# Kernel optimization log

Measured on AMD Instinct MI355X. Metric: run time of the kernel, lower is better.

Reference implementation:

```python
import jax, jax.numpy as jnp
import numpy as np

TEMP = 0.1
COEFF = 0.5
WARMUP = 0
S = 32 * 32  # hardcoded in the torch module


def _l2n(x, axis):
    # matches F.normalize(p=2, eps=1e-12)
    n = jnp.linalg.norm(x, axis=axis, keepdims=True)
    return x / jnp.maximum(n, 1e-12)


def _ce_first_class(pos, neg):
    # cross-entropy with label 0 on logits = [pos | neg] / T
    logits = jnp.concatenate([pos, neg], axis=1) / TEMP
    return jnp.mean(jax.nn.logsumexp(logits, axis=1) - logits[:, 0])


def _dense_losses(q_of, q_x, k_of, k_x, k_avg_dense):
    # q_of,k_of: (B,d,S) normalized; q_x,k_x: (B,C,S) normalized; k_avg_dense: (B,C) UN-normalized (torch bug preserved)
    B, C, _ = q_x.shape
    sim = jnp.einsum('bds,bdt->bst', q_of, k_of)          # (B,S,S)
    ind = jnp.argmax(sim, axis=2)                          # (B,S)
    idxg = jnp.take_along_axis(k_x, jnp.broadcast_to(ind[:, None, :], k_x.shape), axis=2)
    idxg = jax.lax.stop_gradient(idxg)                     # computed under torch.no_grad
    l_pos = jnp.sum(q_x * idxg, axis=1).reshape(-1, 1)     # (B*S,1)
    qf = jnp.transpose(q_x, (0, 2, 1)).reshape(-1, C)      # (B*S,C)
    l_neg_full = qf @ k_avg_dense.T                        # (B*S,B)
    # static mask: row n excludes column n // S
    base = np.stack([np.delete(np.arange(B), i) for i in range(B)])  # (B,B-1)
    neg_cols = jnp.asarray(np.repeat(base, S, axis=0))     # (B*S,B-1)
    l_neg = jnp.take_along_axis(l_neg_full, neg_cols, axis=1)
    return l_pos, l_neg


def _forward(original_features_q, avgpooled_global_q, x_q, avgpooled_dense_q,
             original_features_k, avgpooled_global_k, x_k, avgpooled_dense_k, epoch):
    of = jnp.concatenate([original_features_q, original_features_k], axis=0)
    ag = jnp.concatenate([avgpooled_global_q, avgpooled_global_k], axis=0)
    x = jnp.concatenate([x_q, x_k], axis=0)
    ad = jnp.concatenate([avgpooled_dense_q, avgpooled_dense_k], axis=0)

    # global InfoNCE
    agn = _l2n(ag, 1)
    sim = agn @ agn.T                                      # (2B,2B)
    n2 = sim.shape[0]
    B = n2 // 2
    rows = np.arange(n2)
    pos_cols = (rows + B) % n2
    pos = sim[jnp.asarray(rows), jnp.asarray(pos_cols)][:, None]
    neg_cols = np.stack([np.setdiff1d(rows, [i, pos_cols[i]]) for i in range(n2)])  # (2B,2B-2)
    neg = jnp.take_along_axis(sim, jnp.asarray(neg_cols), axis=1)
    global_loss = _ce_first_class(pos, neg)

    # dense InfoNCE
    b, d, h, w = of.shape
    of = _l2n(of.reshape(b, d, h * w), 1)
    xn = _l2n(x, 1)
    q_of, k_of = of[:b // 2], of[b // 2:]
    q_x, k_x = xn[:b // 2], xn[b // 2:]
    q_ad, k_ad = ad[:b // 2], ad[b // 2:]  # NOTE: un-normalized, matching the torch code
    p1, n1 = _dense_losses(q_of, q_x, k_of, k_x, k_ad)
    p2, n2_ = _dense_losses(k_of, k_x, q_of, q_x, q_ad)
    dense_loss = _ce_first_class(jnp.concatenate([p1, p2], axis=0),
                                 jnp.concatenate([n1, n2_], axis=0))

    if epoch > WARMUP:
        return COEFF * global_loss + (1.0 - COEFF) * dense_loss
    return global_loss


def setup_inputs() -> dict:
    key = jax.random.key(0)
    ks = jax.random.split(key, 8)
    B, d, C, h, w = 64, 256, 128, 32, 32
    return {
        'original_features_q': jax.random.normal(ks[0], (B, d, h, w), jnp.float32),
        'avgpooled_global_q': jax.random.normal(ks[1], (B, C), jnp.float32),
        'x_q': jax.random.normal(ks[2], (B, C, h * w), jnp.float32),
        'avgpooled_dense_q': jax.random.normal(ks[3], (B, C), jnp.float32),
        'original_features_k': jax.random.normal(ks[4], (B, d, h, w), jnp.float32),
        'avgpooled_global_k': jax.random.normal(ks[5], (B, C), jnp.float32),
        'x_k': jax.random.normal(ks[6], (B, C, h * w), jnp.float32),
        'avgpooled_dense_k': jax.random.normal(ks[7], (B, C), jnp.float32),
        'epoch': 5,
    }


def reference(original_features_q, avgpooled_global_q, x_q, avgpooled_dense_q,
              original_features_k, avgpooled_global_k, x_k, avgpooled_dense_k, epoch):
    return _forward(original_features_q, avgpooled_global_q, x_q, avgpooled_dense_q,
                    original_features_k, avgpooled_global_k, x_k, avgpooled_dense_k, epoch)
```

## Files before the change

### kernel.cpp

```cpp
#include <hip/hip_runtime.h>
#include <math.h>

#define TEMP_INV 10.0f

typedef unsigned long long u64;
typedef __attribute__((ext_vector_type(8))) __bf16 bf16x8;
typedef __attribute__((ext_vector_type(4))) float f32x4;

__device__ inline unsigned fkey(float v) {
  unsigned u = __float_as_uint(v);
  return (u & 0x80000000u) ? ~u : (u | 0x80000000u);
}
__device__ inline u64 packvi(float v, unsigned idx) {
  return ((u64)fkey(v) << 32) | (u64)(0xFFFFFFFFu - idx);
}

__device__ __forceinline__ void async_copy16(const void* gp, void* lp) {
  __builtin_amdgcn_global_load_lds(
      (__attribute__((address_space(1))) void*)(unsigned long long)gp,
      (__attribute__((address_space(3))) void*)(unsigned long long)lp,
      16, 0, 0);
}

__global__ __launch_bounds__(256) void kcvt(const float* __restrict__ ofq,
                                            const float* __restrict__ ofk,
                                            __bf16* __restrict__ ofT,
                                            float* __restrict__ of_invn) {
  int s0 = blockIdx.x * 32, b = blockIdx.y;
  const float* src = (b < 64) ? (ofq + (size_t)b * 262144) : (ofk + (size_t)(b - 64) * 262144);
  __shared__ __bf16 T[32][36];
  __shared__ float R[8][32];
  int t = threadIdx.x;
  int dd = t >> 5, ss = t & 31;
  int wr = t >> 3, wd = t & 7;
  float ssq = 0.f;
  __bf16* out = ofT + (size_t)b * 262144 + (size_t)s0 * 256;
  for (int d0 = 0; d0 < 256; d0 += 32) {
    float v[4];
#pragma unroll
    for (int it = 0; it < 4; ++it) {
      int d = d0 + dd + 8 * it;
      v[it] = src[(size_t)d * 1024 + s0 + ss];
      ssq += v[it] * v[it];
    }
    __syncthreads();
#pragma unroll
    for (int it = 0; it < 4; ++it) T[ss][dd + 8 * it] = (__bf16)v[it];
    __syncthreads();
    *(uint2*)(out + (size_t)wr * 256 + d0 + wd * 4) = *(const uint2*)(&T[wr][wd * 4]);
  }
  R[dd][ss] = ssq;
  __syncthreads();
  if (t < 32) {
    float a = 0.f;
#pragma unroll
    for (int r = 0; r < 8; ++r) a += R[r][t];
    of_invn[b * 1024 + s0 + t] = 1.0f / fmaxf(sqrtf(a), 1e-12f);
  }
}

__global__ void kprep(const float* __restrict__ xq, const float* __restrict__ xk,
                      float* __restrict__ x_invn,
                      const float* __restrict__ adq, const float* __restrict__ adk,
                      float* __restrict__ adt) {
  if (blockIdx.x < 512) {
    int idx = blockIdx.x * 256 + threadIdx.x;
    int b = idx >> 10, s = idx & 1023;
    const float* src = (b < 64) ? (xq + (size_t)b * 131072) : (xk + (size_t)(b - 64) * 131072);
    float acc = 0.f;
#pragma unroll 8
    for (int c = 0; c < 128; ++c) { float v = src[c * 1024 + s]; acc += v * v; }
    x_invn[idx] = 1.0f / fmaxf(sqrtf(acc), 1e-12f);
  } else {
    int i = (blockIdx.x - 512) * 256 + threadIdx.x;
    int dir = i >> 13, r = i & 8191;
    int j = r >> 7, c = r & 127;
    const float* ad = dir == 0 ? adk : adq;
    adt[dir * 8192 + c * 64 + j] = ad[j * 128 + c];
  }
}

__global__ __launch_bounds__(256) void ksim(
    const __bf16* __restrict__ ofT, const float* __restrict__ of_invn,
    u64* __restrict__ best_row, u64* __restrict__ best_col) {
  int b = blockIdx.z;
  int s0 = blockIdx.x * 128, t0 = blockIdx.y * 128;
  const __bf16* Ag = ofT + (size_t)b * 262144;
  const __bf16* Bg = ofT + (size_t)(b + 64) * 262144;
  __shared__ __bf16 As[2][4096];
  __shared__ __bf16 Bs[2][4096];
  __shared__ float siq[128], sik[128];
  int t = threadIdx.x;
  if (t < 128) siq[t] = of_invn[b * 1024 + s0 + t];
  else sik[t - 128] = of_invn[65536 + b * 1024 + t0 + (t - 128)];

  f32x4 acc[4][4];
#pragma unroll
  for (int i = 0; i < 4; ++i)
#pragma unroll
    for (int j = 0; j < 4; ++j) acc[i][j] = (f32x4)(0.f);

  int lane = t & 63, w = t >> 6;
  int lc = lane & 15, q = lane >> 4;
  int wm = w & 1, wn = w >> 1;

  int aoff[4], boff[4];
#pragma unroll
  for (int i = 0; i < 4; ++i) {
    int mr = wm * 64 + i * 16 + lc;
    aoff[i] = mr * 32 + (((q + mr + (mr >> 2)) & 3) << 3);
    int nc = wn * 64 + i * 16 + lc;
    boff[i] = nc * 32 + (((q + nc + (nc >> 2)) & 3) << 3);
  }

  int kp = t & 3;
  int mA0 = t >> 2, lgA0 = (kp - mA0 - (mA0 >> 2)) & 3;
  int mA1 = 64 + (t >> 2), lgA1 = (kp - mA1 - (mA1 >> 2)) & 3;

  async_copy16(Ag + (size_t)(s0 + mA0) * 256 + lgA0 * 8, (char*)&As[0][0] + t * 16);
  async_copy16(Bg + (size_t)(t0 + mA0) * 256 + lgA0 * 8, (char*)&Bs[0][0] + t * 16);
  async_copy16(Ag + (size_t)(s0 + mA1) * 256 + lgA1 * 8, (char*)&As[0][0] + 4096 + t * 16);
  async_copy16(Bg + (size_t)(t0 + mA1) * 256 + lgA1 * 8, (char*)&Bs[0][0] + 4096 + t * 16);
  __syncthreads();

  for (int it = 0; it < 8; ++it) {
    int buf = it & 1;
    bf16x8 af[4], bfr[4];
#pragma unroll
    for (int i = 0; i < 4; ++i) af[i] = *(const bf16x8*)(&As[buf][0] + aoff[i]);
#pragma unroll
    for (int j = 0; j < 4; ++j) bfr[j] = *(const bf16x8*)(&Bs[buf][0] + boff[j]);
    if (it < 7) {
      int k0 = (it + 1) * 32;
      async_copy16(Ag + (size_t)(s0 + mA0) * 256 + k0 + lgA0 * 8, (char*)&As[buf ^ 1][0] + t * 16);
      async_copy16(Bg + (size_t)(t0 + mA0) * 256 + k0 + lgA0 * 8, (char*)&Bs[buf ^ 1][0] + t * 16);
      async_copy16(Ag + (size_t)(s0 + mA1) * 256 + k0 + lgA1 * 8, (char*)&As[buf ^ 1][0] + 4096 + t * 16);
      async_copy16(Bg + (size_t)(t0 + mA1) * 256 + k0 + lgA1 * 8, (char*)&Bs[buf ^ 1][0] + 4096 + t * 16);
    }
#pragma unroll
    for (int i = 0; i < 4; ++i)
#pragma unroll
      for (int j = 0; j < 4; ++j)
        acc[i][j] = __builtin_amdgcn_mfma_f32_16x16x32_bf16(af[i], bfr[j], acc[i][j], 0, 0, 0);
    __syncthreads();
  }

  float sk[4], sq[16];
#pragma unroll
  for (int j = 0; j < 4; ++j) sk[j] = sik[wn * 64 + j * 16 + lc];
#pragma unroll
  for (int i = 0; i < 4; ++i)
#pragma unroll
    for (int e = 0; e < 4; ++e) sq[i * 4 + e] = siq[wm * 64 + i * 16 + q * 4 + e];

  u64* browb = best_row + (size_t)b * 1024 + s0;
  u64* bcolb = best_col + (size_t)b * 1024 + t0;

#pragma unroll
  for (int i = 0; i < 4; ++i) {
#pragma unroll
    for (int e = 0; e < 4; ++e) {
      float v[4];
#pragma unroll
      for (int j = 0; j < 4; ++j) v[j] = acc[i][j][e] * sk[j];
      float vb = fmaxf(fmaxf(v[0], v[1]), fmaxf(v[2], v[3]));
#pragma unroll
      for (int mask = 1; mask <= 8; mask <<= 1) vb = fmaxf(vb, __shfl_xor(vb, mask));
      unsigned ib = 0xFFFFFFFFu;
#pragma unroll
      for (int j = 0; j < 4; ++j) {
        unsigned cand = (v[j] == vb) ? (unsigned)(t0 + wn * 64 + j * 16 + lc) : 0xFFFFFFFFu;
        ib = min(ib, cand);
      }
#pragma unroll
      for (int mask = 1; mask <= 8; mask <<= 1) ib = min(ib, __shfl_xor(ib, mask));
      if (lc == 0)
        atomicMax(browb + wm * 64 + i * 16 + q * 4 + e, ((u64)fkey(vb) << 32) | (u64)(0xFFFFFFFFu - ib));
    }
  }

#pragma unroll
  for (int j = 0; j < 4; ++j) {
    float cb = -INFINITY;
#pragma unroll
    for (int i = 0; i < 4; ++i)
#pragma unroll
      for (int e = 0; e < 4; ++e) cb = fmaxf(cb, acc[i][j][e] * sq[i * 4 + e]);
    cb = fmaxf(cb, __shfl_xor(cb, 16));
    cb = fmaxf(cb, __shfl_xor(cb, 32));
    unsigned ib = 0xFFFFFFFFu;
#pragma unroll
    for (int i = 0; i < 4; ++i)
#pragma unroll
      for (int e = 0; e < 4; ++e) {
        float m2 = acc[i][j][e] * sq[i * 4 + e];
        unsigned cand = (m2 == cb) ? (unsigned)(s0 + wm * 64 + i * 16 + q * 4 + e) : 0xFFFFFFFFu;
        ib = min(ib, cand);
      }
    ib = min(ib, __shfl_xor(ib, 16));
    ib = min(ib, __shfl_xor(ib, 32));
    if (lane < 16)
      atomicMax(bcolb + wn * 64 + j * 16 + lane, ((u64)fkey(cb) << 32) | (u64)(0xFFFFFFFFu - ib));
  }
}

__global__ __launch_bounds__(1024) void kpos(
    const float* __restrict__ xq, const float* __restrict__ xk,
    const float* __restrict__ x_invn,
    const u64* __restrict__ best_row, const u64* __restrict__ best_col,
    float* __restrict__ posl) {
  int b = blockIdx.x, dir = blockIdx.y;
  const float* xsrc = dir == 0 ? xq : xk;
  const float* xdst = dir == 0 ? xk : xq;
  const float* inv_src = x_invn + (dir ? 65536 : 0);
  const float* inv_dst = x_invn + (dir ? 0 : 65536);
  const u64* best = dir == 0 ? best_row : best_col;

  __shared__ float xrow[8][1024];
  __shared__ float sdinv[1024];
  int t = threadIdx.x;
  sdinv[t] = inv_dst[b * 1024 + t];
  u64 p = best[(size_t)b * 1024 + t];
  int sidx = (int)(0xFFFFFFFFu - (unsigned)(p & 0xFFFFFFFFull));
  const float* xsb = xsrc + (size_t)b * 131072;
  const float* xdb = xdst + (size_t)b * 131072;
  float acc = 0.f;
  for (int c0 = 0; c0 < 128; c0 += 8) {
    __syncthreads();
#pragma unroll
    for (int qq = 0; qq < 2; ++qq)
      ((float4*)xrow)[t + 1024 * qq] = ((const float4*)(xdb + (size_t)c0 * 1024))[t + 1024 * qq];
    __syncthreads();
#pragma unroll
    for (int cc = 0; cc < 8; ++cc)
      acc += xsb[(size_t)(c0 + cc) * 1024 + t] * xrow[cc][sidx];
  }
  posl[dir * 65536 + b * 1024 + t] = acc * inv_src[b * 1024 + t] * sdinv[sidx] * TEMP_INV;
}

__global__ __launch_bounds__(256) void kneg(
    const float* __restrict__ xq, const float* __restrict__ xk,
    const float* __restrict__ x_invn,
    const float* __restrict__ adt, const float* __restrict__ posl,
    float* __restrict__ dsum) {
  int st = blockIdx.x, b = blockIdx.y, dir = blockIdx.z;
  const float* xsrc = dir == 0 ? xq : xk;
  const float* inv_src = x_invn + (dir ? 65536 : 0);
  const float* Bt = adt + dir * 8192;

  __shared__ float As2[64][64];
  __shared__ float Bs2[128][64];
  __shared__ float red[16];

  int tid = threadIdx.x;
  int tx = tid & 15, ty = tid >> 4;
  int s0 = st * 64;

#pragma unroll
  for (int qq = 0; qq < 8; ++qq)
    reinterpret_cast<float4*>(Bs2)[tid + 256 * qq] =
        reinterpret_cast<const float4*>(Bt)[tid + 256 * qq];

  float acc[4][4];
#pragma unroll
  for (int i = 0; i < 4; ++i)
#pragma unroll
    for (int j = 0; j < 4; ++j) acc[i][j] = 0.f;

  int lm = tid & 63, lk = tid >> 6;
  float sinv = inv_src[b * 1024 + s0 + lm];
  const float* xb = xsrc + (size_t)b * 131072;

  for (int k0 = 0; k0 < 128; k0 += 64) {
#pragma unroll
    for (int r = 0; r < 16; ++r) {
      int kk = lk + 4 * r;
      As2[kk][lm] = xb[(k0 + kk) * 1024 + s0 + lm] * sinv;
    }
    __syncthreads();
#pragma unroll
    for (int kk = 0; kk < 64; ++kk) {
      float4 av = *reinterpret_cast<const float4*>(&As2[kk][ty * 4]);
      float4 bv = *reinterpret_cast<const float4*>(&Bs2[k0 + kk][tx * 4]);
      float a[4] = {av.x, av.y, av.z, av.w};
      float bb[4] = {bv.x, bv.y, bv.z, bv.w};
#pragma unroll
      for (int i = 0; i < 4; ++i)
#pragma unroll
        for (int j = 0; j < 4; ++j) acc[i][j] += a[i] * bb[j];
    }
    __syncthreads();
  }

  float lsum = 0.f;
#pragma unroll
  for (int i = 0; i < 4; ++i) {
    int s = s0 + ty * 4 + i;
    float pos = posl[dir * 65536 + b * 1024 + s];
    float lg[4];
    float mloc = -INFINITY;
#pragma unroll
    for (int j = 0; j < 4; ++j) {
      int jg = tx * 4 + j;
      lg[j] = (jg == b) ? -INFINITY : acc[i][j] * TEMP_INV;
      mloc = fmaxf(mloc, lg[j]);
    }
#pragma unroll
    for (int mask = 1; mask <= 8; mask <<= 1) mloc = fmaxf(mloc, __shfl_xor(mloc, mask));
    float m = fmaxf(mloc, pos);
    float e = 0.f;
#pragma unroll
    for (int j = 0; j < 4; ++j) e += __expf(lg[j] - m);
#pragma unroll
    for (int mask = 1; mask <= 8; mask <<= 1) e += __shfl_xor(e, mask);
    if (tx == 0) lsum += m + __logf(e + __expf(pos - m)) - pos;
  }
  if (tx == 0) red[ty] = lsum;
  __syncthreads();
  if (tid == 0) {
    float v = 0.f;
#pragma unroll
    for (int r = 0; r < 16; ++r) v += red[r];
    atomicAdd(dsum, v);
  }
}

__global__ void kglobal(const float* __restrict__ agq, const float* __restrict__ agk,
                        float* __restrict__ gsum) {
  __shared__ float logits[128];
  __shared__ float rinv[128];
  int i = blockIdx.x, j = threadIdx.x;
  const float* rowi = (i < 64) ? (agq + i * 128) : (agk + (i - 64) * 128);
  const float* rowj = (j < 64) ? (agq + j * 128) : (agk + (j - 64) * 128);
  float dot = 0.f, nj = 0.f;
#pragma unroll 8
  for (int c = 0; c < 128; ++c) { float a = rowi[c], bb = rowj[c]; dot += a * bb; nj += bb * bb; }
  rinv[j] = 1.0f / fmaxf(sqrtf(nj), 1e-12f);
  __syncthreads();
  logits[j] = dot * rinv[i] * rinv[j] * TEMP_INV;
  __syncthreads();
  if (j == 0) {
    int pos = (i + 64) & 127;
    float m = -INFINITY;
    for (int t = 0; t < 128; ++t) if (t != i) m = fmaxf(m, logits[t]);
    float e = 0.f;
    for (int t = 0; t < 128; ++t) if (t != i) e += __expf(logits[t] - m);
    atomicAdd(gsum, m + __logf(e) - logits[pos]);
  }
}

__global__ void kfinal(const float* __restrict__ gsum, const float* __restrict__ dsum,
                       const int* __restrict__ epoch, float* __restrict__ out) {
  if (threadIdx.x == 0) {
    float g = gsum[0] / 128.0f;
    float dn = dsum[0] / 131072.0f;
    out[0] = (epoch[0] > 0) ? (0.5f * g + 0.5f * dn) : g;
  }
}

extern "C" void kernel_launch(void* const* d_in, const int* in_sizes, int n_in,
                              void* d_out, int out_size, void* d_ws, size_t ws_size,
                              hipStream_t stream) {
  const float* ofq = (const float*)d_in[0];
  const float* agq = (const float*)d_in[1];
  const float* xq  = (const float*)d_in[2];
  const float* adq = (const float*)d_in[3];
  const float* ofk = (const float*)d_in[4];
  const float* agk = (const float*)d_in[5];
  const float* xk  = (const float*)d_in[6];
  const float* adk = (const float*)d_in[7];
  const int* epoch = (const int*)d_in[8];
  float* out = (float*)d_out;

  char* wsb = (char*)d_ws;
  __bf16* ofT = (__bf16*)wsb;
  u64* best_row = (u64*)(wsb + 67108864);
  u64* best_col = best_row + 65536;
  float* gsum = (float*)(best_col + 65536);
  float* dsum = gsum + 1;
  float* posl = dsum + 1;
  float* x_invn  = posl + 131072;
  float* of_invn = x_invn + 131072;
  float* adt = of_invn + 131072;

  hipMemsetAsync(best_row, 0, 65536ull * 8 * 2 + 8, stream);

  dim3 gc(32, 128);
  kcvt<<<gc, 256, 0, stream>>>(ofq, ofk, ofT, of_invn);
  kprep<<<576, 256, 0, stream>>>(xq, xk, x_invn, adq, adk, adt);
  kglobal<<<128, 128, 0, stream>>>(agq, agk, gsum);

  dim3 gs(8, 8, 64);
  ksim<<<gs, 256, 0, stream>>>(ofT, of_invn, best_row, best_col);

  dim3 gp(64, 2);
  kpos<<<gp, 1024, 0, stream>>>(xq, xk, x_invn, best_row, best_col, posl);

  dim3 gn(16, 64, 2);
  kneg<<<gn, 256, 0, stream>>>(xq, xk, x_invn, adt, posl, dsum);

  kfinal<<<1, 1, 0, stream>>>(gsum, dsum, epoch, out);
}
```

Measured before the change: 421.9 us.

## Enlarge similarity GEMM tiles to 256x256 with XOR-swizzled 64-wide K stages

```diff
diff --git a/kernel.cpp b/kernel.cpp
--- a/kernel.cpp
+++ b/kernel.cpp
@@ -10,9 +10,6 @@
 __device__ inline unsigned fkey(float v) {
   unsigned u = __float_as_uint(v);
   return (u & 0x80000000u) ? ~u : (u | 0x80000000u);
-}
-__device__ inline u64 packvi(float v, unsigned idx) {
-  return ((u64)fkey(v) << 32) | (u64)(0xFFFFFFFFu - idx);
 }
 
 __device__ __forceinline__ void async_copy16(const void* gp, void* lp) {
@@ -80,84 +77,94 @@
   }
 }
 
-__global__ __launch_bounds__(256) void ksim(
+__global__ __launch_bounds__(512, 2) void ksim(
     const __bf16* __restrict__ ofT, const float* __restrict__ of_invn,
     u64* __restrict__ best_row, u64* __restrict__ best_col) {
   int b = blockIdx.z;
-  int s0 = blockIdx.x * 128, t0 = blockIdx.y * 128;
+  int s0 = blockIdx.x * 256, t0 = blockIdx.y * 256;
   const __bf16* Ag = ofT + (size_t)b * 262144;
   const __bf16* Bg = ofT + (size_t)(b + 64) * 262144;
-  __shared__ __bf16 As[2][4096];
-  __shared__ __bf16 Bs[2][4096];
-  __shared__ float siq[128], sik[128];
+  __shared__ __bf16 As[2][16384];
+  __shared__ __bf16 Bs[2][16384];
+
   int t = threadIdx.x;
-  if (t < 128) siq[t] = of_invn[b * 1024 + s0 + t];
-  else sik[t - 128] = of_invn[65536 + b * 1024 + t0 + (t - 128)];
-
-  f32x4 acc[4][4];
-#pragma unroll
-  for (int i = 0; i < 4; ++i)
-#pragma unroll
-    for (int j = 0; j < 4; ++j) acc[i][j] = (f32x4)(0.f);
-
   int lane = t & 63, w = t >> 6;
   int lc = lane & 15, q = lane >> 4;
-  int wm = w & 1, wn = w >> 1;
-
-  int aoff[4], boff[4];
-#pragma unroll
-  for (int i = 0; i < 4; ++i) {
-    int mr = wm * 64 + i * 16 + lc;
-    aoff[i] = mr * 32 + (((q + mr + (mr >> 2)) & 3) << 3);
-    int nc = wn * 64 + i * 16 + lc;
-    boff[i] = nc * 32 + (((q + nc + (nc >> 2)) & 3) << 3);
-  }
-
-  int kp = t & 3;
-  int mA0 = t >> 2, lgA0 = (kp - mA0 - (mA0 >> 2)) & 3;
-  int mA1 = 64 + (t >> 2), lgA1 = (kp - mA1 - (mA1 >> 2)) & 3;
-
-  async_copy16(Ag + (size_t)(s0 + mA0) * 256 + lgA0 * 8, (char*)&As[0][0] + t * 16);
-  async_copy16(Bg + (size_t)(t0 + mA0) * 256 + lgA0 * 8, (char*)&Bs[0][0] + t * 16);
-  async_copy16(Ag + (size_t)(s0 + mA1) * 256 + lgA1 * 8, (char*)&As[0][0] + 4096 + t * 16);
-  async_copy16(Bg + (size_t)(t0 + mA1) * 256 + lgA1 * 8, (char*)&Bs[0][0] + 4096 + t * 16);
+  int wm = w >> 2, wn = w & 3;
+
+  f32x4 acc[8][4];
+#pragma unroll
+  for (int i = 0; i < 8; ++i)
+#pragma unroll
+    for (int j = 0; j < 4; ++j) acc[i][j] = (f32x4)(0.f);
+
+  int aoff[8], boff[4];
+#pragma unroll
+  for (int i = 0; i < 8; ++i) {
+    int mr = wm * 128 + i * 16 + lc;
+    aoff[i] = mr * 64 + ((q ^ (mr & 7)) << 3);
+  }
+#pragma unroll
+  for (int j = 0; j < 4; ++j) {
+    int nc = wn * 64 + j * 16 + lc;
+    boff[j] = nc * 64 + ((q ^ (nc & 7)) << 3);
+  }
+
+  int ms = t >> 3, gphys = t & 7;
+  int lg = gphys ^ (ms & 7);
+  size_t aSrc = (size_t)(s0 + ms) * 256 + lg * 8;
+  size_t bSrc = (size_t)(t0 + ms) * 256 + lg * 8;
+
+  auto STAGE = [&](int bufn, int k0) {
+    char* aL = (char*)&As[bufn][0] + t * 16;
+    char* bL = (char*)&Bs[bufn][0] + t * 16;
+#pragma unroll
+    for (int c = 0; c < 4; ++c) {
+      async_copy16(Ag + aSrc + (size_t)c * 16384 + k0, aL + c * 8192);
+      async_copy16(Bg + bSrc + (size_t)c * 16384 + k0, bL + c * 8192);
+    }
+  };
+
+  STAGE(0, 0);
   __syncthreads();
 
-  for (int it = 0; it < 8; ++it) {
+  for (int it = 0; it < 4; ++it) {
     int buf = it & 1;
-    bf16x8 af[4], bfr[4];
-#pragma unroll
-    for (int i = 0; i < 4; ++i) af[i] = *(const bf16x8*)(&As[buf][0] + aoff[i]);
-#pragma unroll
-    for (int j = 0; j < 4; ++j) bfr[j] = *(const bf16x8*)(&Bs[buf][0] + boff[j]);
-    if (it < 7) {
-      int k0 = (it + 1) * 32;
-      async_copy16(Ag + (size_t)(s0 + mA0) * 256 + k0 + lgA0 * 8, (char*)&As[buf ^ 1][0] + t * 16);
-      async_copy16(Bg + (size_t)(t0 + mA0) * 256 + k0 + lgA0 * 8, (char*)&Bs[buf ^ 1][0] + t * 16);
-      async_copy16(Ag + (size_t)(s0 + mA1) * 256 + k0 + lgA1 * 8, (char*)&As[buf ^ 1][0] + 4096 + t * 16);
-      async_copy16(Bg + (size_t)(t0 + mA1) * 256 + k0 + lgA1 * 8, (char*)&Bs[buf ^ 1][0] + 4096 + t * 16);
-    }
-#pragma unroll
-    for (int i = 0; i < 4; ++i)
-#pragma unroll
-      for (int j = 0; j < 4; ++j)
-        acc[i][j] = __builtin_amdgcn_mfma_f32_16x16x32_bf16(af[i], bfr[j], acc[i][j], 0, 0, 0);
-    __syncthreads();
-  }
-
-  float sk[4], sq[16];
-#pragma unroll
-  for (int j = 0; j < 4; ++j) sk[j] = sik[wn * 64 + j * 16 + lc];
-#pragma unroll
-  for (int i = 0; i < 4; ++i)
-#pragma unroll
-    for (int e = 0; e < 4; ++e) sq[i * 4 + e] = siq[wm * 64 + i * 16 + q * 4 + e];
+    if (it < 3) STAGE(buf ^ 1, (it + 1) * 64);
+#pragma unroll
+    for (int kk = 0; kk < 2; ++kk) {
+      int kx = kk << 5;
+      bf16x8 af[8], bfr[4];
+#pragma unroll
+      for (int i = 0; i < 8; ++i) af[i] = *(const bf16x8*)(&As[buf][0] + (aoff[i] ^ kx));
+#pragma unroll
+      for (int j = 0; j < 4; ++j) bfr[j] = *(const bf16x8*)(&Bs[buf][0] + (boff[j] ^ kx));
+      __builtin_amdgcn_s_setprio(1);
+#pragma unroll
+      for (int i = 0; i < 8; ++i)
+#pragma unroll
+        for (int j = 0; j < 4; ++j)
+          acc[i][j] = __builtin_amdgcn_mfma_f32_16x16x32_bf16(af[i], bfr[j], acc[i][j], 0, 0, 0);
+      __builtin_amdgcn_s_setprio(0);
+    }
+    __syncthreads();
+  }
+
+  float sk[4];
+#pragma unroll
+  for (int j = 0; j < 4; ++j) sk[j] = of_invn[65536 + b * 1024 + t0 + wn * 64 + j * 16 + lc];
+  float sq[32];
+#pragma unroll
+  for (int i = 0; i < 8; ++i)
+#pragma unroll
+    for (int e = 0; e < 4; ++e)
+      sq[i * 4 + e] = of_invn[b * 1024 + s0 + wm * 128 + i * 16 + q * 4 + e];
 
   u64* browb = best_row + (size_t)b * 1024 + s0;
   u64* bcolb = best_col + (size_t)b * 1024 + t0;
 
 #pragma unroll
-  for (int i = 0; i < 4; ++i) {
+  for (int i = 0; i < 8; ++i) {
 #pragma unroll
     for (int e = 0; e < 4; ++e) {
       float v[4];
@@ -175,7 +182,8 @@
 #pragma unroll
       for (int mask = 1; mask <= 8; mask <<= 1) ib = min(ib, __shfl_xor(ib, mask));
       if (lc == 0)
-        atomicMax(browb + wm * 64 + i * 16 + q * 4 + e, ((u64)fkey(vb) << 32) | (u64)(0xFFFFFFFFu - ib));
+        atomicMax(browb + wm * 128 + i * 16 + q * 4 + e,
+                  ((u64)fkey(vb) << 32) | (u64)(0xFFFFFFFFu - ib));
     }
   }
 
@@ -183,24 +191,25 @@
   for (int j = 0; j < 4; ++j) {
     float cb = -INFINITY;
 #pragma unroll
-    for (int i = 0; i < 4; ++i)
+    for (int i = 0; i < 8; ++i)
 #pragma unroll
       for (int e = 0; e < 4; ++e) cb = fmaxf(cb, acc[i][j][e] * sq[i * 4 + e]);
     cb = fmaxf(cb, __shfl_xor(cb, 16));
     cb = fmaxf(cb, __shfl_xor(cb, 32));
     unsigned ib = 0xFFFFFFFFu;
 #pragma unroll
-    for (int i = 0; i < 4; ++i)
+    for (int i = 0; i < 8; ++i)
 #pragma unroll
       for (int e = 0; e < 4; ++e) {
         float m2 = acc[i][j][e] * sq[i * 4 + e];
-        unsigned cand = (m2 == cb) ? (unsigned)(s0 + wm * 64 + i * 16 + q * 4 + e) : 0xFFFFFFFFu;
+        unsigned cand = (m2 == cb) ? (unsigned)(s0 + wm * 128 + i * 16 + q * 4 + e) : 0xFFFFFFFFu;
         ib = min(ib, cand);
       }
     ib = min(ib, __shfl_xor(ib, 16));
     ib = min(ib, __shfl_xor(ib, 32));
     if (lane < 16)
-      atomicMax(bcolb + wn * 64 + j * 16 + lane, ((u64)fkey(cb) << 32) | (u64)(0xFFFFFFFFu - ib));
+      atomicMax(bcolb + wn * 64 + j * 16 + lane,
+                ((u64)fkey(cb) << 32) | (u64)(0xFFFFFFFFu - ib));
   }
 }
 
@@ -390,8 +399,8 @@
   kprep<<<576, 256, 0, stream>>>(xq, xk, x_invn, adq, adk, adt);
   kglobal<<<128, 128, 0, stream>>>(agq, agk, gsum);
 
-  dim3 gs(8, 8, 64);
-  ksim<<<gs, 256, 0, stream>>>(ofT, of_invn, best_row, best_col);
+  dim3 gs(4, 4, 64);
+  ksim<<<gs, 512, 0, stream>>>(ofT, of_invn, best_row, best_col);
 
   dim3 gp(64, 2);
   kpos<<<gp, 1024, 0, stream>>>(xq, xk, x_invn, best_row, best_col, posl);
```

Measured after the change: 403.6 us. 1.05x faster.

## Load MFMA operands directly from global into registers, drop LDS staging in ksim

Applied to the files above, without the earlier changes.

```diff
diff --git a/kernel.cpp b/kernel.cpp
--- a/kernel.cpp
+++ b/kernel.cpp
@@ -10,16 +10,6 @@
 __device__ inline unsigned fkey(float v) {
   unsigned u = __float_as_uint(v);
   return (u & 0x80000000u) ? ~u : (u | 0x80000000u);
-}
-__device__ inline u64 packvi(float v, unsigned idx) {
-  return ((u64)fkey(v) << 32) | (u64)(0xFFFFFFFFu - idx);
-}
-
-__device__ __forceinline__ void async_copy16(const void* gp, void* lp) {
-  __builtin_amdgcn_global_load_lds(
-      (__attribute__((address_space(1))) void*)(unsigned long long)gp,
-      (__attribute__((address_space(3))) void*)(unsigned long long)lp,
-      16, 0, 0);
 }
 
 __global__ __launch_bounds__(256) void kcvt(const float* __restrict__ ofq,
@@ -80,78 +70,63 @@
   }
 }
 
-__global__ __launch_bounds__(256) void ksim(
+__global__ __launch_bounds__(256, 3) void ksim(
     const __bf16* __restrict__ ofT, const float* __restrict__ of_invn,
     u64* __restrict__ best_row, u64* __restrict__ best_col) {
   int b = blockIdx.z;
   int s0 = blockIdx.x * 128, t0 = blockIdx.y * 128;
   const __bf16* Ag = ofT + (size_t)b * 262144;
   const __bf16* Bg = ofT + (size_t)(b + 64) * 262144;
-  __shared__ __bf16 As[2][4096];
-  __shared__ __bf16 Bs[2][4096];
-  __shared__ float siq[128], sik[128];
+
   int t = threadIdx.x;
-  if (t < 128) siq[t] = of_invn[b * 1024 + s0 + t];
-  else sik[t - 128] = of_invn[65536 + b * 1024 + t0 + (t - 128)];
-
-  f32x4 acc[4][4];
-#pragma unroll
-  for (int i = 0; i < 4; ++i)
-#pragma unroll
-    for (int j = 0; j < 4; ++j) acc[i][j] = (f32x4)(0.f);
-
   int lane = t & 63, w = t >> 6;
   int lc = lane & 15, q = lane >> 4;
-  int wm = w & 1, wn = w >> 1;
-
-  int aoff[4], boff[4];
+  int wm = w >> 1, wn = w & 1;
+
+  const __bf16* Aw = Ag + (size_t)(s0 + wm * 64 + lc) * 256 + q * 8;
+  const __bf16* Bw = Bg + (size_t)(t0 + wn * 64 + lc) * 256 + q * 8;
+
+  f32x4 acc[4][4];
+#pragma unroll
+  for (int i = 0; i < 4; ++i)
+#pragma unroll
+    for (int j = 0; j < 4; ++j) acc[i][j] = (f32x4)(0.f);
+
+  bf16x8 af[2][4], bfr[2][4];
 #pragma unroll
   for (int i = 0; i < 4; ++i) {
-    int mr = wm * 64 + i * 16 + lc;
-    aoff[i] = mr * 32 + (((q + mr + (mr >> 2)) & 3) << 3);
-    int nc = wn * 64 + i * 16 + lc;
-    boff[i] = nc * 32 + (((q + nc + (nc >> 2)) & 3) << 3);
-  }
-
-  int kp = t & 3;
-  int mA0 = t >> 2, lgA0 = (kp - mA0 - (mA0 >> 2)) & 3;
-  int mA1 = 64 + (t >> 2), lgA1 = (kp - mA1 - (mA1 >> 2)) & 3;
-
-  async_copy16(Ag + (size_t)(s0 + mA0) * 256 + lgA0 * 8, (char*)&As[0][0] + t * 16);
-  async_copy16(Bg + (size_t)(t0 + mA0) * 256 + lgA0 * 8, (char*)&Bs[0][0] + t * 16);
-  async_copy16(Ag + (size_t)(s0 + mA1) * 256 + lgA1 * 8, (char*)&As[0][0] + 4096 + t * 16);
-  async_copy16(Bg + (size_t)(t0 + mA1) * 256 + lgA1 * 8, (char*)&Bs[0][0] + 4096 + t * 16);
-  __syncthreads();
-
+    af[0][i] = *(const bf16x8*)(Aw + (size_t)i * 4096);
+    bfr[0][i] = *(const bf16x8*)(Bw + (size_t)i * 4096);
+  }
+
+#pragma unroll
   for (int it = 0; it < 8; ++it) {
-    int buf = it & 1;
-    bf16x8 af[4], bfr[4];
-#pragma unroll
-    for (int i = 0; i < 4; ++i) af[i] = *(const bf16x8*)(&As[buf][0] + aoff[i]);
-#pragma unroll
-    for (int j = 0; j < 4; ++j) bfr[j] = *(const bf16x8*)(&Bs[buf][0] + boff[j]);
+    const int cur = it & 1;
     if (it < 7) {
-      int k0 = (it + 1) * 32;
-      async_copy16(Ag + (size_t)(s0 + mA0) * 256 + k0 + lgA0 * 8, (char*)&As[buf ^ 1][0] + t * 16);
-      async_copy16(Bg + (size_t)(t0 + mA0) * 256 + k0 + lgA0 * 8, (char*)&Bs[buf ^ 1][0] + t * 16);
-      async_copy16(Ag + (size_t)(s0 + mA1) * 256 + k0 + lgA1 * 8, (char*)&As[buf ^ 1][0] + 4096 + t * 16);
-      async_copy16(Bg + (size_t)(t0 + mA1) * 256 + k0 + lgA1 * 8, (char*)&Bs[buf ^ 1][0] + 4096 + t * 16);
+      int k1 = (it + 1) * 32;
+#pragma unroll
+      for (int i = 0; i < 4; ++i) {
+        af[cur ^ 1][i] = *(const bf16x8*)(Aw + (size_t)i * 4096 + k1);
+        bfr[cur ^ 1][i] = *(const bf16x8*)(Bw + (size_t)i * 4096 + k1);
+      }
     }
 #pragma unroll
     for (int i = 0; i < 4; ++i)
 #pragma unroll
       for (int j = 0; j < 4; ++j)
-        acc[i][j] = __builtin_amdgcn_mfma_f32_16x16x32_bf16(af[i], bfr[j], acc[i][j], 0, 0, 0);
-    __syncthreads();
-  }
-
-  float sk[4], sq[16];
-#pragma unroll
-  for (int j = 0; j < 4; ++j) sk[j] = sik[wn * 64 + j * 16 + lc];
+        acc[i][j] =
+            __builtin_amdgcn_mfma_f32_16x16x32_bf16(af[cur][i], bfr[cur][j], acc[i][j], 0, 0, 0);
+  }
+
+  float sk[4];
+#pragma unroll
+  for (int j = 0; j < 4; ++j) sk[j] = of_invn[65536 + b * 1024 + t0 + wn * 64 + j * 16 + lc];
+  float sq[16];
 #pragma unroll
   for (int i = 0; i < 4; ++i)
 #pragma unroll
-    for (int e = 0; e < 4; ++e) sq[i * 4 + e] = siq[wm * 64 + i * 16 + q * 4 + e];
+    for (int e = 0; e < 4; ++e)
+      sq[i * 4 + e] = of_invn[b * 1024 + s0 + wm * 64 + i * 16 + q * 4 + e];
 
   u64* browb = best_row + (size_t)b * 1024 + s0;
   u64* bcolb = best_col + (size_t)b * 1024 + t0;
@@ -175,7 +150,8 @@
 #pragma unroll
       for (int mask = 1; mask <= 8; mask <<= 1) ib = min(ib, __shfl_xor(ib, mask));
       if (lc == 0)
-        atomicMax(browb + wm * 64 + i * 16 + q * 4 + e, ((u64)fkey(vb) << 32) | (u64)(0xFFFFFFFFu - ib));
+        atomicMax(browb + wm * 64 + i * 16 + q * 4 + e,
+                  ((u64)fkey(vb) << 32) | (u64)(0xFFFFFFFFu - ib));
     }
   }
 
@@ -200,7 +176,8 @@
     ib = min(ib, __shfl_xor(ib, 16));
     ib = min(ib, __shfl_xor(ib, 32));
     if (lane < 16)
-      atomicMax(bcolb + wn * 64 + j * 16 + lane, ((u64)fkey(cb) << 32) | (u64)(0xFFFFFFFFu - ib));
+      atomicMax(bcolb + wn * 64 + j * 16 + lane,
+                ((u64)fkey(cb) << 32) | (u64)(0xFFFFFFFFu - ib));
   }
 }
 
```

Measured after the change: 471.8 us. +11.8%, slower.
